# Kernel optimization log

Measured on AMD Instinct MI355X. Metric: run time of the kernel, lower is better.

The kernel has to match this reference:

```python
import jax, jax.numpy as jnp
import numpy as np

N_NODES = 16500   # 100 battles x 165 hexes
N_EDGES = 100000  # per link type
K = 3             # number of link types (HeteroConv branches)
C_IN, C_HID, C_OUT = 170, 256, 256
GEN_EPS = 1e-7    # GENConv eps
BN_EPS = 1e-5     # BatchNorm1d eps


def setup_inputs() -> dict:
    key = jax.random.key(0)
    ki = iter(jax.random.split(key, 32))
    inp = {}
    inp["x"] = jax.random.normal(next(ki), (N_NODES, C_IN), jnp.float32)
    inp["edge_index"] = jax.random.randint(next(ki), (K, 2, N_EDGES), 0, N_NODES, dtype=jnp.int32)
    inp["edge_attr"] = jax.random.normal(next(ki), (K, N_EDGES, 1), jnp.float32)

    def uni(k, fan_in, shape):
        b = float(1.0 / np.sqrt(fan_in))
        return jax.random.uniform(k, shape, jnp.float32, -b, b)

    dims = [(C_IN, C_HID), (C_HID, C_HID), (C_HID, C_OUT)]
    for l, (ci, co) in enumerate(dims):
        inp[f"We{l}"] = uni(next(ki), 1, (K, 1, ci))          # edge encoder Linear(1, ci)
        inp[f"be{l}"] = jnp.zeros((K, ci), jnp.float32)
        inp[f"Wa{l}"] = uni(next(ki), ci, (K, ci, 2 * ci))     # MLP layer 1 (expansion=2)
        inp[f"ba{l}"] = jnp.zeros((K, 2 * ci), jnp.float32)
        inp[f"g{l}"] = jnp.ones((K, 2 * ci), jnp.float32)      # BatchNorm gamma
        inp[f"bt{l}"] = jnp.zeros((K, 2 * ci), jnp.float32)    # BatchNorm beta
        inp[f"Wb{l}"] = uni(next(ki), 2 * ci, (K, 2 * ci, co)) # MLP layer 2
        inp[f"bb{l}"] = jnp.zeros((K, co), jnp.float32)
    return inp


def _genconv(x, src, dst, ea, We, be, Wa, ba, g, bt, Wb, bb):
    """PyG GENConv (aggr='softmax', t=1, eps=1e-7, norm='batch') with self loops."""
    n = x.shape[0]
    loops = jnp.arange(n, dtype=src.dtype)
    src = jnp.concatenate([src, loops])
    dst = jnp.concatenate([dst, loops])
    ea = jnp.concatenate([ea, jnp.ones((n, ea.shape[1]), ea.dtype)], axis=0)
    e = ea @ We + be                           # [E+N, ci] edge encoder
    msg = jax.nn.relu(x[src] + e) + GEN_EPS    # [E+N, ci] message
    # per-destination, per-channel segment softmax aggregation
    mx = jax.ops.segment_max(msg, dst, num_segments=n)
    w = jnp.exp(msg - mx[dst])
    den = jax.ops.segment_sum(w, dst, num_segments=n)
    aggr = jax.ops.segment_sum(msg * w, dst, num_segments=n) / den
    out = aggr + x                             # residual with root node
    # MLP: Linear -> BatchNorm(train stats) -> ReLU -> Linear
    h = out @ Wa + ba
    mu = h.mean(axis=0)
    var = ((h - mu) ** 2).mean(axis=0)
    h = (h - mu) * jax.lax.rsqrt(var + BN_EPS) * g + bt
    h = jax.nn.relu(h)
    return h @ Wb + bb


_conv_k = jax.vmap(_genconv, in_axes=(None, 0, 0, 0, 0, 0, 0, 0, 0, 0, 0, 0))


def _forward(x, edge_index, edge_attr, layers):
    h = x
    for i, p in enumerate(layers):
        # HeteroConv: run GENConv per link type, sum-aggregate over types
        h = _conv_k(h, edge_index[:, 0], edge_index[:, 1], edge_attr, *p).sum(axis=0)
        if i < len(layers) - 1:
            h = jax.nn.leaky_relu(h, 0.01)
    return h


def reference(x, edge_index, edge_attr,
              We0, be0, Wa0, ba0, g0, bt0, Wb0, bb0,
              We1, be1, Wa1, ba1, g1, bt1, Wb1, bb1,
              We2, be2, Wa2, ba2, g2, bt2, Wb2, bb2):
    layers = [(We0, be0, Wa0, ba0, g0, bt0, Wb0, bb0),
              (We1, be1, Wa1, ba1, g1, bt1, Wb1, bb1),
              (We2, be2, Wa2, ba2, g2, bt2, Wb2, bb2)]
    return _forward(x, edge_index, edge_attr, layers)
```

## Files before the change

### kernel.cpp

```cpp
#include <hip/hip_runtime.h>
#include <math.h>

#define NN 16500
#define NP 16512
#define NE 100000
#define KT 3

typedef __attribute__((ext_vector_type(8))) short bf8_t;
typedef __attribute__((ext_vector_type(4))) float f4_t;

__device__ __forceinline__ unsigned short f2bf(float f) {
    unsigned int u = __float_as_uint(f);
    u += 0x7fffu + ((u >> 16) & 1u);
    return (unsigned short)(u >> 16);
}
__device__ __forceinline__ float bf2f(unsigned short h) {
    return __uint_as_float(((unsigned int)h) << 16);
}
__device__ __forceinline__ void gload16(unsigned short* lds, const unsigned short* g) {
    __builtin_amdgcn_global_load_lds(
        (const __attribute__((address_space(1))) void*)g,
        (__attribute__((address_space(3))) void*)lds, 16, 0, 0);
}


__global__ void deg_kernel(const int* __restrict__ ei, int* __restrict__ deg) {
    int t = blockIdx.x * blockDim.x + threadIdx.x;
    if (t >= KT * NE) return;
    int k = t / NE, e = t - k * NE;
    int d = ei[k * 2 * NE + NE + e];
    atomicAdd(&deg[k * NN + d], 1);
}

__global__ void scan_kernel(const int* __restrict__ deg, int* __restrict__ offs,
                            int* __restrict__ cursor) {
    int k = blockIdx.x;
    const int* dg = deg + k * NN;
    int* of = offs + k * (NN + 1);
    int* cu = cursor + k * NN;
    __shared__ int part[256];
    int tid = threadIdx.x;
    const int chunk = (NN + 255) / 256;
    int s0 = tid * chunk, s1 = min(NN, s0 + chunk);
    if (s0 > s1) s0 = s1;
    int sum = 0;
    for (int i = s0; i < s1; ++i) sum += dg[i];
    part[tid] = sum;
    __syncthreads();
    for (int off = 1; off < 256; off <<= 1) {
        int v = part[tid];
        int vp = (tid >= off) ? part[tid - off] : 0;
        __syncthreads();
        part[tid] = v + vp;
        __syncthreads();
    }
    int run = (tid == 0) ? 0 : part[tid - 1];
    for (int i = s0; i < s1; ++i) {
        of[i] = run; cu[i] = run;
        run += dg[i];
    }
    if (tid == 255) of[NN] = run;
}

__global__ void scatter_kernel(const int* __restrict__ ei, int* __restrict__ cursor,
                               int* __restrict__ eids) {
    int t = blockIdx.x * blockDim.x + threadIdx.x;
    if (t >= KT * NE) return;
    int k = t / NE, e = t - k * NE;
    int d = ei[k * 2 * NE + NE + e];
    int pos = atomicAdd(&cursor[k * NN + d], 1);
    eids[k * NE + pos] = e;
}


template<int CI, bool BF16X>
__device__ __forceinline__ void loadrow4(float out[4], const void* xv, int s, int c0) {
    if (BF16X) {
        const unsigned short* xb = (const unsigned short*)xv;
        uint2 u = *(const uint2*)(xb + (size_t)s * CI + c0);
        out[0] = bf2f((unsigned short)(u.x & 0xffffu));
        out[1] = bf2f((unsigned short)(u.x >> 16));
        out[2] = bf2f((unsigned short)(u.y & 0xffffu));
        out[3] = bf2f((unsigned short)(u.y >> 16));
    } else {
        const float* p = (const float*)xv + (size_t)s * CI + c0;
        if (c0 + 4 <= CI) {
            float2 ab = *(const float2*)p;
            float2 cd = *(const float2*)(p + 2);
            out[0] = ab.x; out[1] = ab.y; out[2] = cd.x; out[3] = cd.y;
        } else {
            #pragma unroll
            for (int e = 0; e < 4; ++e) out[e] = (c0 + e < CI) ? p[e] : 0.f;
        }
    }
}

template<int CI, bool BF16X>
__global__ __launch_bounds__(256) void aggr_kernel(
    const void* __restrict__ xv, const int* __restrict__ ei,
    const float* __restrict__ ea_all, const int* __restrict__ offs_all,
    const int* __restrict__ eids_all, const float* __restrict__ We_all,
    const float* __restrict__ be_all,
    unsigned short* __restrict__ out_hi)
{
    constexpr int KP = (CI + 31) / 32 * 32;
    int k = blockIdx.y;
    int wv = threadIdx.x >> 6, lane = threadIdx.x & 63;
    int d = blockIdx.x * 4 + wv;
    int c0 = lane * 4;
    unsigned short* o = out_hi + (size_t)k * NP * KP;
    if (d >= NN) {
        if (c0 < KP) { uint2 z = {0u, 0u}; *(uint2*)(o + (size_t)d * KP + c0) = z; }
        return;
    }
    const int*   src  = ei + (size_t)k * 2 * NE;
    const float* ea   = ea_all + (size_t)k * NE;
    const int*   offs = offs_all + k * (NN + 1);
    const int*   eids = eids_all + (size_t)k * NE;
    const float* We   = We_all + (size_t)k * CI;
    const float* be   = be_all + (size_t)k * CI;

    constexpr bool ACT_ALL = (64 * 4 == KP) && (CI == KP);
    bool act = ACT_ALL || (c0 < CI);
    float w[4], b[4], xd[4] = {0.f, 0.f, 0.f, 0.f};
    #pragma unroll
    for (int e = 0; e < 4; ++e) {
        bool a = (c0 + e) < CI;
        w[e] = a ? We[c0 + e] : 0.f;
        b[e] = a ? be[c0 + e] : 0.f;
    }
    if (act) loadrow4<CI, BF16X>(xd, xv, d, c0);
    #pragma unroll
    for (int e = 0; e < 4; ++e) if ((c0 + e) >= CI) xd[e] = 0.f;

    float m[4], den[4], num[4];
    #pragma unroll
    for (int e = 0; e < 4; ++e) {
        float mg = fmaxf(xd[e] + w[e] + b[e], 0.f);
        m[e] = mg; den[e] = 1.f; num[e] = mg;
    }

    auto step = [&](const float xc[4], float a) {
        #pragma unroll
        for (int e = 0; e < 4; ++e) {
            float t = xc[e] + fmaf(a, w[e], b[e]);
            float mg = fmaxf(t, 0.f);
            float nm = fmaxf(m[e], mg);
            float mn = fminf(m[e], mg);
            float ex = __expf(mn - nm);
            bool keep = m[e] >= mg;
            float e0 = keep ? 1.f : ex;
            float e1 = keep ? ex : 1.f;
            den[e] = fmaf(den[e], e0, e1);
            num[e] = fmaf(num[e], e0, mg * e1);
            m[e] = nm;
        }
    };

    int start = offs[d], end = offs[d + 1];
    for (int base = start; base < end; base += 64) {
        int cnt = min(64, end - base);
        int sv = 0; float av = 0.f;
        if (lane < cnt) {
            int e2 = eids[base + lane];
            sv = src[e2];
            av = ea[e2];
        }
        float x0[4] = {0.f,0.f,0.f,0.f}, x1[4] = {0.f,0.f,0.f,0.f};
        {
            int sA = __shfl(sv, 0);
            if (act) loadrow4<CI, BF16X>(x0, xv, sA, c0);
        }
        if (cnt > 1) {
            int sB = __shfl(sv, 1);
            if (act) loadrow4<CI, BF16X>(x1, xv, sB, c0);
        }
        int j = 0;
        for (; j + 1 < cnt; j += 2) {
            float a0 = __shfl(av, j), a1 = __shfl(av, j + 1);
            float tA[4] = {x0[0], x0[1], x0[2], x0[3]};
            float tB[4] = {x1[0], x1[1], x1[2], x1[3]};
            if (j + 2 < cnt) {
                int sn = __shfl(sv, j + 2);
                if (act) loadrow4<CI, BF16X>(x0, xv, sn, c0);
            }
            if (j + 3 < cnt) {
                int sn = __shfl(sv, j + 3);
                if (act) loadrow4<CI, BF16X>(x1, xv, sn, c0);
            }
            step(tA, a0);
            step(tB, a1);
        }
        if (j < cnt) {
            float a0 = __shfl(av, j);
            step(x0, a0);
        }
    }
    if (c0 < KP) {
        unsigned short r[4];
        #pragma unroll
        for (int e = 0; e < 4; ++e) {
            float v = ((c0 + e) < CI) ? (num[e] / den[e] + xd[e]) : 0.f;
            r[e] = f2bf(v);
        }
        uint2 pk = {(unsigned)r[0] | ((unsigned)r[1] << 16),
                    (unsigned)r[2] | ((unsigned)r[3] << 16)};
        *(uint2*)(o + (size_t)d * KP + c0) = pk;
    }
}


struct SplitJob { const float* W; unsigned short* out; int kdim, ndim, np_, kp; };
struct SplitJobs { SplitJob j[6]; };

__global__ void split_all_kernel(SplitJobs jobs) {
    SplitJob jb = jobs.j[blockIdx.z];
    int idx = blockIdx.x * 256 + threadIdx.x;
    int total = KT * jb.np_ * jb.kp;
    if (idx >= total) return;
    int k = idx / (jb.np_ * jb.kp);
    int rem = idx - k * jb.np_ * jb.kp;
    int n = rem / jb.kp;
    int kk = rem - n * jb.kp;
    float v = (n < jb.ndim && kk < jb.kdim) ? jb.W[((size_t)k * jb.kdim + kk) * jb.ndim + n] : 0.f;
    jb.out[idx] = f2bf(v);
}


__global__ __launch_bounds__(256, 3) void gemm1_mfma(
    const unsigned short* __restrict__ A_hi,
    const unsigned short* __restrict__ B_hi,
    const float* __restrict__ bias_all, unsigned short* __restrict__ C_all,
    float* __restrict__ psum,
    int KP, int ldc, int Mv, int Nv)
{
    __shared__ unsigned short Ah[128 * 32];
    __shared__ unsigned short Bh[128 * 32];

    int z = blockIdx.z;
    int gxT = gridDim.x, gyT = gridDim.y;
    int NHP = gxT * 128;
    const unsigned short* Ahg = A_hi + (size_t)z * NP * KP;
    const unsigned short* Bhg = B_hi + (size_t)z * NHP * KP;
    const float* bias = bias_all + (size_t)z * Nv;
    unsigned short* C = C_all + (size_t)z * NP * ldc;

    int tid = threadIdx.x;
    int w = tid >> 6, l = tid & 63;
    int bm = blockIdx.y * 128, bn = blockIdx.x * 128;
    int lane15 = l & 15, quad = l >> 4;
    int wm = (w >> 1) * 64, wn = (w & 1) * 64;
    int srow = l & 15;
    int scol = (l >> 4) * 8;

    f4_t acc[4][4];
    #pragma unroll
    for (int i = 0; i < 4; ++i)
        #pragma unroll
        for (int j = 0; j < 4; ++j) { f4_t zz = {0.f,0.f,0.f,0.f}; acc[i][j] = zz; }

    size_t aoff0 = (size_t)(bm + 32 * w +  0 + srow) * KP + scol;
    size_t aoff1 = (size_t)(bm + 32 * w + 16 + srow) * KP + scol;
    size_t boff0 = (size_t)(bn + 32 * w +  0 + srow) * KP + scol;
    size_t boff1 = (size_t)(bn + 32 * w + 16 + srow) * KP + scol;
    int rb0 = 32 * w, rb1 = 32 * w + 16;
    int ta = (w >> 1) * 4, tb = (w & 1) * 4;

    for (int k0 = 0; k0 < KP; k0 += 32) {
        gload16(&Ah[rb0 * 32], Ahg + aoff0 + k0);
        gload16(&Ah[rb1 * 32], Ahg + aoff1 + k0);
        gload16(&Bh[rb0 * 32], Bhg + boff0 + k0);
        gload16(&Bh[rb1 * 32], Bhg + boff1 + k0);
        __syncthreads();

        bf8_t fa[4], fb[4];
        #pragma unroll
        for (int i = 0; i < 4; ++i) {
            fa[i] = *(const bf8_t*)&Ah[(ta + i) * 512 + l * 8];
            fb[i] = *(const bf8_t*)&Bh[(tb + i) * 512 + l * 8];
        }
        #pragma unroll
        for (int i = 0; i < 4; ++i)
            #pragma unroll
            for (int j = 0; j < 4; ++j)
                acc[i][j] = __builtin_amdgcn_mfma_f32_16x16x32_bf16(fa[i], fb[j], acc[i][j], 0, 0, 0);
        __syncthreads();
    }

    #pragma unroll
    for (int j = 0; j < 4; ++j) {
        int c = bn + wn + j * 16 + lane15;
        float bc = (c < Nv) ? bias[c] : 0.f;
        float s1 = 0.f, s2 = 0.f;
        #pragma unroll
        for (int i = 0; i < 4; ++i) {
            #pragma unroll
            for (int r5 = 0; r5 < 4; ++r5) {
                int r = bm + wm + i * 16 + quad * 4 + r5;
                float v = acc[i][j][r5] + bc;
                unsigned short q = f2bf(v);
                if (r < Mv && c < Nv) C[(size_t)r * ldc + c] = q;
                bool ok = (r < NN) && (c < Nv);
                float vq = ok ? bf2f(q) : 0.f;
                s1 += vq;
                s2 = fmaf(vq, vq, s2);
            }
        }
        s1 += __shfl_xor(s1, 16); s2 += __shfl_xor(s2, 16);
        s1 += __shfl_xor(s1, 32); s2 += __shfl_xor(s2, 32);
        if (quad == 0) {
            int wrow = w >> 1;
            int col = wn + j * 16 + lane15;
            size_t o = ((((size_t)z * gyT + blockIdx.y) * gxT + blockIdx.x) * 2 + wrow) * 256 + col * 2;
            float2 st = {s1, s2};
            *(float2*)&psum[o] = st;
        }
    }
}


__global__ __launch_bounds__(512) void finalize_kernel(
    const float* __restrict__ psum,
    const float* __restrict__ g_all, const float* __restrict__ bt_all,
    float* __restrict__ scale_all, float* __restrict__ shift_all,
    int hid, int gxT)
{
    int z = blockIdx.x;
    int c = threadIdx.x;
    if (c >= hid) return;
    int gx = c >> 7, col = c & 127;
    double s1 = 0.0, s2 = 0.0;
    for (int gy = 0; gy < NP / 128; ++gy) {
        size_t base = (((size_t)z * (NP / 128) + gy) * gxT + gx) * 2 * 256 + col * 2;
        float2 a  = *(const float2*)&psum[base];
        float2 b2 = *(const float2*)&psum[base + 256];
        s1 += (double)a.x + b2.x;
        s2 += (double)a.y + b2.y;
    }
    double mu = s1 / NN;
    double var = s2 / NN - mu * mu;
    if (var < 0.0) var = 0.0;
    float rs = (float)(1.0 / sqrt(var + 1e-5));
    float sc = rs * g_all[(size_t)z * hid + c];
    scale_all[(size_t)z * 512 + c] = sc;
    shift_all[(size_t)z * 512 + c] = bt_all[(size_t)z * hid + c] - (float)mu * sc;
}


__global__ __launch_bounds__(256, 3) void gemm2_mfma(
    const unsigned short* __restrict__ h_all, const float* __restrict__ scale_all,
    const float* __restrict__ shift_all,
    const unsigned short* __restrict__ B_hi,
    float* __restrict__ P_all, int KP, int hid, int Mv)
{
    __shared__ unsigned short Ah[128 * 32];
    __shared__ unsigned short Bh[128 * 32];

    int z = blockIdx.z;
    const unsigned short* hz = h_all + (size_t)z * NP * KP;
    const float* scl = scale_all + (size_t)z * 512;
    const float* shf = shift_all + (size_t)z * 512;
    const unsigned short* Bhg = B_hi + (size_t)z * 256 * KP;
    float* P = P_all + (size_t)z * NP * 256;

    int tid = threadIdx.x;
    int w = tid >> 6, l = tid & 63;
    int bm = blockIdx.y * 128, bn = blockIdx.x * 128;
    int lane15 = l & 15, quad = l >> 4;
    int wm = (w >> 1) * 64, wn = (w & 1) * 64;
    int srow = l & 15, scol = (l >> 4) * 8;

    f4_t acc[4][4];
    #pragma unroll
    for (int i = 0; i < 4; ++i)
        #pragma unroll
        for (int j = 0; j < 4; ++j) { f4_t zz = {0.f,0.f,0.f,0.f}; acc[i][j] = zz; }

    size_t boff0 = (size_t)(bn + 32 * w +  0 + srow) * KP + scol;
    size_t boff1 = (size_t)(bn + 32 * w + 16 + srow) * KP + scol;
    int rb0 = 32 * w, rb1 = 32 * w + 16;
    int ta = (w >> 1) * 4, tb = (w & 1) * 4;

    for (int k0 = 0; k0 < KP; k0 += 32) {
        gload16(&Bh[rb0 * 32], Bhg + boff0 + k0);
        gload16(&Bh[rb1 * 32], Bhg + boff1 + k0);

        #pragma unroll
        for (int sseg = 0; sseg < 2; ++sseg) {
            int L = sseg * 256 + tid;
            int chunk = (L >> 4) & 3;
            int grow = ((L >> 6) << 4) + (L & 15);
            int c = k0 + chunk * 8;
            uint4 hv = *(const uint4*)(hz + (size_t)(bm + grow) * KP + c);
            float4 s0 = *(const float4*)(scl + c);
            float4 s1 = *(const float4*)(scl + c + 4);
            float4 t0 = *(const float4*)(shf + c);
            float4 t1 = *(const float4*)(shf + c + 4);
            unsigned int uu[4] = {hv.x, hv.y, hv.z, hv.w};
            float ss[8] = {s0.x, s0.y, s0.z, s0.w, s1.x, s1.y, s1.z, s1.w};
            float tt[8] = {t0.x, t0.y, t0.z, t0.w, t1.x, t1.y, t1.z, t1.w};
            bf8_t hi8;
            #pragma unroll
            for (int e = 0; e < 8; ++e) {
                unsigned short hb = (e & 1) ? (unsigned short)(uu[e >> 1] >> 16)
                                            : (unsigned short)(uu[e >> 1] & 0xffffu);
                float x = bf2f(hb);
                float val = (c + e < hid) ? fmaxf(fmaf(x, ss[e], tt[e]), 0.f) : 0.f;
                hi8[e] = (short)f2bf(val);
            }
            *(bf8_t*)&Ah[L * 8] = hi8;
        }
        __syncthreads();

        bf8_t fa[4], fb[4];
        #pragma unroll
        for (int i = 0; i < 4; ++i) {
            fa[i] = *(const bf8_t*)&Ah[(ta + i) * 512 + l * 8];
            fb[i] = *(const bf8_t*)&Bh[(tb + i) * 512 + l * 8];
        }
        #pragma unroll
        for (int i = 0; i < 4; ++i)
            #pragma unroll
            for (int j = 0; j < 4; ++j)
                acc[i][j] = __builtin_amdgcn_mfma_f32_16x16x32_bf16(fa[i], fb[j], acc[i][j], 0, 0, 0);
        __syncthreads();
    }

    #pragma unroll
    for (int i = 0; i < 4; ++i)
        #pragma unroll
        for (int j = 0; j < 4; ++j) {
            int c = bn + wn + j * 16 + lane15;
            #pragma unroll
            for (int r5 = 0; r5 < 4; ++r5) {
                int r = bm + wm + i * 16 + quad * 4 + r5;
                if (r < Mv)
                    P[(size_t)r * 256 + c] = acc[i][j][r5];
            }
        }
}


__global__ __launch_bounds__(256) void reduce_kernel(
    const float* __restrict__ P, const float* __restrict__ bb,
    float* __restrict__ outf, unsigned short* __restrict__ outb,
    int leaky, int as_bf16)
{
    int idx = blockIdx.x * 256 + threadIdx.x;
    if (idx >= NN * 64) return;
    int r = idx >> 6, c = (idx & 63) * 4;
    const float4 p0 = *(const float4*)&P[((size_t)0 * NP + r) * 256 + c];
    const float4 p1 = *(const float4*)&P[((size_t)1 * NP + r) * 256 + c];
    const float4 p2 = *(const float4*)&P[((size_t)2 * NP + r) * 256 + c];
    const float4 b0 = *(const float4*)&bb[c];
    const float4 b1 = *(const float4*)&bb[256 + c];
    const float4 b2 = *(const float4*)&bb[512 + c];
    float v[4] = {p0.x + p1.x + p2.x + b0.x + b1.x + b2.x,
                  p0.y + p1.y + p2.y + b0.y + b1.y + b2.y,
                  p0.z + p1.z + p2.z + b0.z + b1.z + b2.z,
                  p0.w + p1.w + p2.w + b0.w + b1.w + b2.w};
    if (leaky) {
        #pragma unroll
        for (int e = 0; e < 4; ++e) v[e] = (v[e] > 0.f) ? v[e] : 0.01f * v[e];
    }
    if (as_bf16) {
        unsigned int o0 = (unsigned int)f2bf(v[0]) | ((unsigned int)f2bf(v[1]) << 16);
        unsigned int o1 = (unsigned int)f2bf(v[2]) | ((unsigned int)f2bf(v[3]) << 16);
        uint2 o = {o0, o1};
        *(uint2*)&outb[(size_t)r * 256 + c] = o;
    } else {
        float4 o = {v[0], v[1], v[2], v[3]};
        *(float4*)&outf[(size_t)r * 256 + c] = o;
    }
}


extern "C" void kernel_launch(void* const* d_in, const int* in_sizes, int n_in,
                              void* d_out, int out_size, void* d_ws, size_t ws_size,
                              hipStream_t stream)
{
    const float* x  = (const float*)d_in[0];
    const int*   ei = (const int*)d_in[1];
    const float* ea = (const float*)d_in[2];

    char* w = (char*)d_ws;
    auto alloc = [&](size_t bytes) {
        char* p = w;
        w += (bytes + 255) & ~(size_t)255;
        return p;
    };
    int* deg    = (int*)alloc((size_t)KT * NN * 4);
    int* offs   = (int*)alloc((size_t)KT * (NN + 1) * 4);
    int* cursor = (int*)alloc((size_t)KT * NN * 4);
    int* eids   = (int*)alloc((size_t)KT * NE * 4);
    unsigned short* a1_hi = (unsigned short*)alloc((size_t)KT * NP * 256 * 2);
    unsigned short* h3 = (unsigned short*)alloc((size_t)KT * NP * 512 * 2);
    float* partial = (float*)alloc((size_t)KT * NP * 256 * 4);
    unsigned short* bta_l[3];
    unsigned short* btb_l[3];
    for (int l = 0; l < 3; ++l) {
        bta_l[l] = (unsigned short*)alloc((size_t)KT * 512 * 256 * 2);
        btb_l[l] = (unsigned short*)alloc((size_t)KT * 256 * 512 * 2);
    }
    float* psum = (float*)alloc((size_t)KT * (NP / 128) * 4 * 2 * 256 * 4);
    float* scale3 = (float*)alloc((size_t)KT * 512 * 4);
    float* shift3 = (float*)alloc((size_t)KT * 512 * 4);
    unsigned short* bufA = (unsigned short*)alloc((size_t)NN * 256 * 2);
    unsigned short* bufB = (unsigned short*)alloc((size_t)NN * 256 * 2);

    hipMemsetAsync(deg, 0, (size_t)KT * NN * 4, stream);
    int net = KT * NE;
    deg_kernel<<<(net + 255) / 256, 256, 0, stream>>>(ei, deg);
    scan_kernel<<<KT, 256, 0, stream>>>(deg, offs, cursor);
    scatter_kernel<<<(net + 255) / 256, 256, 0, stream>>>(ei, cursor, eids);

    SplitJobs jobs;
    int maxtot = 0;
    for (int l = 0; l < 3; ++l) {
        int ci  = (l == 0) ? 170 : 256;
        int KP1 = (ci + 31) / 32 * 32;
        int hid = 2 * ci;
        int NHP = (hid + 127) / 128 * 128;
        int KP2 = (hid + 31) / 32 * 32;
        jobs.j[2 * l]     = { (const float*)d_in[3 + 8 * l + 2], bta_l[l], ci,  hid, NHP, KP1 };
        jobs.j[2 * l + 1] = { (const float*)d_in[3 + 8 * l + 6], btb_l[l], hid, 256, 256, KP2 };
        maxtot = max(maxtot, KT * NHP * KP1);
        maxtot = max(maxtot, KT * 256 * KP2);
    }
    dim3 gsp((maxtot + 255) / 256, 1, 6);
    split_all_kernel<<<gsp, 256, 0, stream>>>(jobs);

    const void* hin = x;
    for (int l = 0; l < 3; ++l) {
        int ci  = (l == 0) ? 170 : 256;
        int KP1 = (ci + 31) / 32 * 32;
        int hid = 2 * ci;
        int NHP = (hid + 127) / 128 * 128;
        int KP2 = (hid + 31) / 32 * 32;
        const float* We = (const float*)d_in[3 + 8 * l + 0];
        const float* be = (const float*)d_in[3 + 8 * l + 1];
        const float* ba = (const float*)d_in[3 + 8 * l + 3];
        const float* g  = (const float*)d_in[3 + 8 * l + 4];
        const float* bt = (const float*)d_in[3 + 8 * l + 5];
        const float* bb = (const float*)d_in[3 + 8 * l + 7];

        dim3 ga(NP / 4, KT);
        if (l == 0)
            aggr_kernel<170, false><<<ga, 256, 0, stream>>>(hin, ei, ea, offs, eids,
                                                            We, be, a1_hi);
        else
            aggr_kernel<256, true><<<ga, 256, 0, stream>>>(hin, ei, ea, offs, eids,
                                                           We, be, a1_hi);

        dim3 g1(NHP / 128, NP / 128, KT);
        gemm1_mfma<<<g1, 256, 0, stream>>>(a1_hi, bta_l[l], ba, h3, psum, KP1, KP2, NN, hid);

        finalize_kernel<<<KT, 512, 0, stream>>>(psum, g, bt, scale3, shift3, hid, NHP / 128);

        dim3 g2(2, NP / 128, KT);
        gemm2_mfma<<<g2, 256, 0, stream>>>(h3, scale3, shift3, btb_l[l],
                                           partial, KP2, hid, NP);

        unsigned short* outb = (l == 0) ? bufA : bufB;
        reduce_kernel<<<(NN * 64 + 255) / 256, 256, 0, stream>>>(
            partial, bb, (float*)d_out, outb, (l < 2) ? 1 : 0, (l < 2) ? 1 : 0);

        hin = (l < 2) ? (const void*)outb : nullptr;
    }
}
```

Baseline: 697.9 us.

## Fuse GEMM2 with cross-type reduction and pre-gather edge sources/attributes

The second MLP GEMM now loops over all three link types inside one block, with 64x256 tiles. It accumulates the HeteroConv sum in registers and applies bias, leaky ReLU and the bf16 cast in the epilogue. This removes the fp32 partial buffer and the separate reduce kernel. The scatter kernel now writes source ids and edge attributes in CSR order, so the aggregation kernel no longer does an indirect eid lookup. In exchange, the GEMM has fewer blocks (NP/64, about 258) and does a serial K loop three times longer, with a software prefetch of the next A chunk. The epilogue also writes scalar 2-byte stores that are poorly coalesced.

```diff
diff --git a/kernel.cpp b/kernel.cpp
--- a/kernel.cpp
+++ b/kernel.cpp
@@ -62,14 +62,16 @@
     if (tid == 255) of[NN] = run;
 }
 
-__global__ void scatter_kernel(const int* __restrict__ ei, int* __restrict__ cursor,
-                               int* __restrict__ eids) {
+__global__ void scatter_kernel(const int* __restrict__ ei, const float* __restrict__ ea,
+                               int* __restrict__ cursor,
+                               int* __restrict__ srcs, float* __restrict__ eas) {
     int t = blockIdx.x * blockDim.x + threadIdx.x;
     if (t >= KT * NE) return;
     int k = t / NE, e = t - k * NE;
     int d = ei[k * 2 * NE + NE + e];
     int pos = atomicAdd(&cursor[k * NN + d], 1);
-    eids[k * NE + pos] = e;
+    srcs[k * NE + pos] = ei[k * 2 * NE + e];
+    eas[k * NE + pos]  = ea[(size_t)k * NE + e];
 }
 
 
@@ -97,10 +99,10 @@
 
 template<int CI, bool BF16X>
 __global__ __launch_bounds__(256) void aggr_kernel(
-    const void* __restrict__ xv, const int* __restrict__ ei,
-    const float* __restrict__ ea_all, const int* __restrict__ offs_all,
-    const int* __restrict__ eids_all, const float* __restrict__ We_all,
-    const float* __restrict__ be_all,
+    const void* __restrict__ xv,
+    const int* __restrict__ srcs_all, const float* __restrict__ eas_all,
+    const int* __restrict__ offs_all,
+    const float* __restrict__ We_all, const float* __restrict__ be_all,
     unsigned short* __restrict__ out_hi)
 {
     constexpr int KP = (CI + 31) / 32 * 32;
@@ -113,10 +115,9 @@
         if (c0 < KP) { uint2 z = {0u, 0u}; *(uint2*)(o + (size_t)d * KP + c0) = z; }
         return;
     }
-    const int*   src  = ei + (size_t)k * 2 * NE;
-    const float* ea   = ea_all + (size_t)k * NE;
+    const int*   srcs = srcs_all + (size_t)k * NE;
+    const float* eas  = eas_all + (size_t)k * NE;
     const int*   offs = offs_all + k * (NN + 1);
-    const int*   eids = eids_all + (size_t)k * NE;
     const float* We   = We_all + (size_t)k * CI;
     const float* be   = be_all + (size_t)k * CI;
 
@@ -162,9 +163,8 @@
         int cnt = min(64, end - base);
         int sv = 0; float av = 0.f;
         if (lane < cnt) {
-            int e2 = eids[base + lane];
-            sv = src[e2];
-            av = ea[e2];
+            sv = srcs[base + lane];
+            av = eas[base + lane];
         }
         float x0[4] = {0.f,0.f,0.f,0.f}, x1[4] = {0.f,0.f,0.f,0.f};
         {
@@ -347,131 +347,117 @@
 }
 
 
-__global__ __launch_bounds__(256, 3) void gemm2_mfma(
+__global__ __launch_bounds__(256) void gemm2_fused(
     const unsigned short* __restrict__ h_all, const float* __restrict__ scale_all,
-    const float* __restrict__ shift_all,
-    const unsigned short* __restrict__ B_hi,
-    float* __restrict__ P_all, int KP, int hid, int Mv)
+    const float* __restrict__ shift_all, const unsigned short* __restrict__ B_all,
+    const float* __restrict__ bb, float* __restrict__ outf,
+    unsigned short* __restrict__ outb, int KP, int hid, int leaky, int as_bf16)
 {
-    __shared__ unsigned short Ah[128 * 32];
-    __shared__ unsigned short Bh[128 * 32];
-
-    int z = blockIdx.z;
-    const unsigned short* hz = h_all + (size_t)z * NP * KP;
-    const float* scl = scale_all + (size_t)z * 512;
-    const float* shf = shift_all + (size_t)z * 512;
-    const unsigned short* Bhg = B_hi + (size_t)z * 256 * KP;
-    float* P = P_all + (size_t)z * NP * 256;
+    __shared__ unsigned short Ah[64 * 32];
+    __shared__ unsigned short Bh[256 * 32];
 
     int tid = threadIdx.x;
     int w = tid >> 6, l = tid & 63;
-    int bm = blockIdx.y * 128, bn = blockIdx.x * 128;
     int lane15 = l & 15, quad = l >> 4;
-    int wm = (w >> 1) * 64, wn = (w & 1) * 64;
+    int bm = blockIdx.x * 64;
+    int wmt = (w >> 1) * 2;
+    int wnt = (w & 1) * 8;
+
+    int ar16   = (tid & 63) >> 2;
+    int achunk = tid & 3;
+    int atile  = tid >> 6;
+    int arow   = atile * 16 + ar16;
+    int aldst  = atile * 512 + (achunk * 16 + ar16) * 8;
+
     int srow = l & 15, scol = (l >> 4) * 8;
 
-    f4_t acc[4][4];
-    #pragma unroll
-    for (int i = 0; i < 4; ++i)
-        #pragma unroll
-        for (int j = 0; j < 4; ++j) { f4_t zz = {0.f,0.f,0.f,0.f}; acc[i][j] = zz; }
-
-    size_t boff0 = (size_t)(bn + 32 * w +  0 + srow) * KP + scol;
-    size_t boff1 = (size_t)(bn + 32 * w + 16 + srow) * KP + scol;
-    int rb0 = 32 * w, rb1 = 32 * w + 16;
-    int ta = (w >> 1) * 4, tb = (w & 1) * 4;
-
-    for (int k0 = 0; k0 < KP; k0 += 32) {
-        gload16(&Bh[rb0 * 32], Bhg + boff0 + k0);
-        gload16(&Bh[rb1 * 32], Bhg + boff1 + k0);
-
-        #pragma unroll
-        for (int sseg = 0; sseg < 2; ++sseg) {
-            int L = sseg * 256 + tid;
-            int chunk = (L >> 4) & 3;
-            int grow = ((L >> 6) << 4) + (L & 15);
-            int c = k0 + chunk * 8;
-            uint4 hv = *(const uint4*)(hz + (size_t)(bm + grow) * KP + c);
-            float4 s0 = *(const float4*)(scl + c);
-            float4 s1 = *(const float4*)(scl + c + 4);
-            float4 t0 = *(const float4*)(shf + c);
-            float4 t1 = *(const float4*)(shf + c + 4);
-            unsigned int uu[4] = {hv.x, hv.y, hv.z, hv.w};
-            float ss[8] = {s0.x, s0.y, s0.z, s0.w, s1.x, s1.y, s1.z, s1.w};
-            float tt[8] = {t0.x, t0.y, t0.z, t0.w, t1.x, t1.y, t1.z, t1.w};
-            bf8_t hi8;
-            #pragma unroll
-            for (int e = 0; e < 8; ++e) {
-                unsigned short hb = (e & 1) ? (unsigned short)(uu[e >> 1] >> 16)
-                                            : (unsigned short)(uu[e >> 1] & 0xffffu);
-                float x = bf2f(hb);
-                float val = (c + e < hid) ? fmaxf(fmaf(x, ss[e], tt[e]), 0.f) : 0.f;
-                hi8[e] = (short)f2bf(val);
-            }
-            *(bf8_t*)&Ah[L * 8] = hi8;
-        }
-        __syncthreads();
-
-        bf8_t fa[4], fb[4];
-        #pragma unroll
-        for (int i = 0; i < 4; ++i) {
-            fa[i] = *(const bf8_t*)&Ah[(ta + i) * 512 + l * 8];
-            fb[i] = *(const bf8_t*)&Bh[(tb + i) * 512 + l * 8];
-        }
-        #pragma unroll
-        for (int i = 0; i < 4; ++i)
-            #pragma unroll
-            for (int j = 0; j < 4; ++j)
-                acc[i][j] = __builtin_amdgcn_mfma_f32_16x16x32_bf16(fa[i], fb[j], acc[i][j], 0, 0, 0);
-        __syncthreads();
-    }
-
-    #pragma unroll
-    for (int i = 0; i < 4; ++i)
-        #pragma unroll
-        for (int j = 0; j < 4; ++j) {
-            int c = bn + wn + j * 16 + lane15;
+    f4_t acc[2][8];
+    #pragma unroll
+    for (int i = 0; i < 2; ++i)
+        #pragma unroll
+        for (int j = 0; j < 8; ++j) { f4_t zz = {0.f,0.f,0.f,0.f}; acc[i][j] = zz; }
+
+    uint4 hp; float4 sp0, sp1, tp0, tp1;
+    {
+        hp = *(const uint4*)(h_all + (size_t)(bm + arow) * KP + achunk * 8);
+        const float* scl = scale_all;
+        const float* shf = shift_all;
+        int c = achunk * 8;
+        sp0 = *(const float4*)(scl + c); sp1 = *(const float4*)(scl + c + 4);
+        tp0 = *(const float4*)(shf + c); tp1 = *(const float4*)(shf + c + 4);
+    }
+
+    for (int z = 0; z < KT; ++z) {
+        const unsigned short* Bz = B_all + (size_t)z * 256 * KP;
+        for (int k0 = 0; k0 < KP; k0 += 32) {
+            #pragma unroll
+            for (int q = 0; q < 4; ++q) {
+                int n = w * 64 + q * 16 + srow;
+                gload16(&Bh[(w * 4 + q) * 512], Bz + (size_t)n * KP + k0 + scol);
+            }
+            uint4 hv = hp;
+            float4 s0 = sp0, s1 = sp1, t0 = tp0, t1 = tp1;
+            int nk = k0 + 32, nz = z;
+            if (nk >= KP) { nk = 0; nz = z + 1; }
+            if (nz < KT) {
+                const unsigned short* hn = h_all + (size_t)nz * NP * KP;
+                hp = *(const uint4*)(hn + (size_t)(bm + arow) * KP + nk + achunk * 8);
+                const float* scl = scale_all + (size_t)nz * 512;
+                const float* shf = shift_all + (size_t)nz * 512;
+                int c = nk + achunk * 8;
+                sp0 = *(const float4*)(scl + c); sp1 = *(const float4*)(scl + c + 4);
+                tp0 = *(const float4*)(shf + c); tp1 = *(const float4*)(shf + c + 4);
+            }
+            {
+                int c = k0 + achunk * 8;
+                unsigned int uu[4] = {hv.x, hv.y, hv.z, hv.w};
+                float ss[8] = {s0.x, s0.y, s0.z, s0.w, s1.x, s1.y, s1.z, s1.w};
+                float tt[8] = {t0.x, t0.y, t0.z, t0.w, t1.x, t1.y, t1.z, t1.w};
+                bf8_t hi8;
+                #pragma unroll
+                for (int e = 0; e < 8; ++e) {
+                    unsigned short hb = (e & 1) ? (unsigned short)(uu[e >> 1] >> 16)
+                                                : (unsigned short)(uu[e >> 1] & 0xffffu);
+                    float x = bf2f(hb);
+                    float val = (c + e < hid) ? fmaxf(fmaf(x, ss[e], tt[e]), 0.f) : 0.f;
+                    hi8[e] = (short)f2bf(val);
+                }
+                *(bf8_t*)&Ah[aldst] = hi8;
+            }
+            __syncthreads();
+
+            bf8_t fa[2], fb[8];
+            #pragma unroll
+            for (int i = 0; i < 2; ++i)
+                fa[i] = *(const bf8_t*)&Ah[(wmt + i) * 512 + l * 8];
+            #pragma unroll
+            for (int j = 0; j < 8; ++j)
+                fb[j] = *(const bf8_t*)&Bh[(wnt + j) * 512 + l * 8];
+            #pragma unroll
+            for (int i = 0; i < 2; ++i)
+                #pragma unroll
+                for (int j = 0; j < 8; ++j)
+                    acc[i][j] = __builtin_amdgcn_mfma_f32_16x16x32_bf16(fa[i], fb[j], acc[i][j], 0, 0, 0);
+            __syncthreads();
+        }
+    }
+
+    #pragma unroll
+    for (int i = 0; i < 2; ++i)
+        #pragma unroll
+        for (int j = 0; j < 8; ++j) {
+            int c = (w & 1) * 128 + j * 16 + lane15;
+            float bc = bb[c] + bb[256 + c] + bb[512 + c];
             #pragma unroll
             for (int r5 = 0; r5 < 4; ++r5) {
-                int r = bm + wm + i * 16 + quad * 4 + r5;
-                if (r < Mv)
-                    P[(size_t)r * 256 + c] = acc[i][j][r5];
-            }
-        }
-}
-
-
-__global__ __launch_bounds__(256) void reduce_kernel(
-    const float* __restrict__ P, const float* __restrict__ bb,
-    float* __restrict__ outf, unsigned short* __restrict__ outb,
-    int leaky, int as_bf16)
-{
-    int idx = blockIdx.x * 256 + threadIdx.x;
-    if (idx >= NN * 64) return;
-    int r = idx >> 6, c = (idx & 63) * 4;
-    const float4 p0 = *(const float4*)&P[((size_t)0 * NP + r) * 256 + c];
-    const float4 p1 = *(const float4*)&P[((size_t)1 * NP + r) * 256 + c];
-    const float4 p2 = *(const float4*)&P[((size_t)2 * NP + r) * 256 + c];
-    const float4 b0 = *(const float4*)&bb[c];
-    const float4 b1 = *(const float4*)&bb[256 + c];
-    const float4 b2 = *(const float4*)&bb[512 + c];
-    float v[4] = {p0.x + p1.x + p2.x + b0.x + b1.x + b2.x,
-                  p0.y + p1.y + p2.y + b0.y + b1.y + b2.y,
-                  p0.z + p1.z + p2.z + b0.z + b1.z + b2.z,
-                  p0.w + p1.w + p2.w + b0.w + b1.w + b2.w};
-    if (leaky) {
-        #pragma unroll
-        for (int e = 0; e < 4; ++e) v[e] = (v[e] > 0.f) ? v[e] : 0.01f * v[e];
-    }
-    if (as_bf16) {
-        unsigned int o0 = (unsigned int)f2bf(v[0]) | ((unsigned int)f2bf(v[1]) << 16);
-        unsigned int o1 = (unsigned int)f2bf(v[2]) | ((unsigned int)f2bf(v[3]) << 16);
-        uint2 o = {o0, o1};
-        *(uint2*)&outb[(size_t)r * 256 + c] = o;
-    } else {
-        float4 o = {v[0], v[1], v[2], v[3]};
-        *(float4*)&outf[(size_t)r * 256 + c] = o;
-    }
+                int r = bm + (w >> 1) * 32 + i * 16 + quad * 4 + r5;
+                if (r >= NN) continue;
+                float v = acc[i][j][r5] + bc;
+                if (leaky) v = (v > 0.f) ? v : 0.01f * v;
+                if (as_bf16) outb[(size_t)r * 256 + c] = f2bf(v);
+                else         outf[(size_t)r * 256 + c] = v;
+            }
+        }
 }
 
 
@@ -492,10 +478,10 @@
     int* deg    = (int*)alloc((size_t)KT * NN * 4);
     int* offs   = (int*)alloc((size_t)KT * (NN + 1) * 4);
     int* cursor = (int*)alloc((size_t)KT * NN * 4);
-    int* eids   = (int*)alloc((size_t)KT * NE * 4);
+    int* srcs   = (int*)alloc((size_t)KT * NE * 4);
+    float* eas  = (float*)alloc((size_t)KT * NE * 4);
     unsigned short* a1_hi = (unsigned short*)alloc((size_t)KT * NP * 256 * 2);
     unsigned short* h3 = (unsigned short*)alloc((size_t)KT * NP * 512 * 2);
-    float* partial = (float*)alloc((size_t)KT * NP * 256 * 4);
     unsigned short* bta_l[3];
     unsigned short* btb_l[3];
     for (int l = 0; l < 3; ++l) {
@@ -512,7 +498,7 @@
     int net = KT * NE;
     deg_kernel<<<(net + 255) / 256, 256, 0, stream>>>(ei, deg);
     scan_kernel<<<KT, 256, 0, stream>>>(deg, offs, cursor);
-    scatter_kernel<<<(net + 255) / 256, 256, 0, stream>>>(ei, cursor, eids);
+    scatter_kernel<<<(net + 255) / 256, 256, 0, stream>>>(ei, ea, cursor, srcs, eas);
 
     SplitJobs jobs;
     int maxtot = 0;
@@ -546,10 +532,10 @@
 
         dim3 ga(NP / 4, KT);
         if (l == 0)
-            aggr_kernel<170, false><<<ga, 256, 0, stream>>>(hin, ei, ea, offs, eids,
+            aggr_kernel<170, false><<<ga, 256, 0, stream>>>(hin, srcs, eas, offs,
                                                             We, be, a1_hi);
         else
-            aggr_kernel<256, true><<<ga, 256, 0, stream>>>(hin, ei, ea, offs, eids,
+            aggr_kernel<256, true><<<ga, 256, 0, stream>>>(hin, srcs, eas, offs,
                                                            We, be, a1_hi);
 
         dim3 g1(NHP / 128, NP / 128, KT);
@@ -557,13 +543,10 @@
 
         finalize_kernel<<<KT, 512, 0, stream>>>(psum, g, bt, scale3, shift3, hid, NHP / 128);
 
-        dim3 g2(2, NP / 128, KT);
-        gemm2_mfma<<<g2, 256, 0, stream>>>(h3, scale3, shift3, btb_l[l],
-                                           partial, KP2, hid, NP);
-
         unsigned short* outb = (l == 0) ? bufA : bufB;
-        reduce_kernel<<<(NN * 64 + 255) / 256, 256, 0, stream>>>(
-            partial, bb, (float*)d_out, outb, (l < 2) ? 1 : 0, (l < 2) ? 1 : 0);
+        gemm2_fused<<<NP / 64, 256, 0, stream>>>(h3, scale3, shift3, btb_l[l], bb,
+                                                 (float*)d_out, outb, KP2, hid,
+                                                 (l < 2) ? 1 : 0, (l < 2) ? 1 : 0);
 
         hin = (l < 2) ? (const void*)outb : nullptr;
     }
```

Measured after the change: 705.9 us. No clear change (+1.1%).

## Pre-gather edge sources/attrs in CSR, deepen aggr prefetch, store partials in bf16

Applied to the files above, without the earlier changes.

The scatter kernel now writes the source index and edge attribute directly into CSR order, so the aggregation kernel reads them contiguously instead of going through an edge-id indirection. The aggregation loop now keeps four neighbour rows in flight per bank, double-buffered across two banks, instead of two. The gemm2 partial outputs are stored as bf16 rather than fp32, halving the traffic to and from reduce_kernel. The extra prefetch depth raises register pressure, and bf16 partials lose precision before the cross-type sum.

```diff
diff --git a/kernel.cpp b/kernel.cpp
--- a/kernel.cpp
+++ b/kernel.cpp
@@ -62,14 +62,16 @@
     if (tid == 255) of[NN] = run;
 }
 
-__global__ void scatter_kernel(const int* __restrict__ ei, int* __restrict__ cursor,
-                               int* __restrict__ eids) {
+__global__ void scatter_kernel(const int* __restrict__ ei, const float* __restrict__ ea,
+                               int* __restrict__ cursor,
+                               int* __restrict__ srcs, float* __restrict__ eas) {
     int t = blockIdx.x * blockDim.x + threadIdx.x;
     if (t >= KT * NE) return;
     int k = t / NE, e = t - k * NE;
     int d = ei[k * 2 * NE + NE + e];
     int pos = atomicAdd(&cursor[k * NN + d], 1);
-    eids[k * NE + pos] = e;
+    srcs[k * NE + pos] = ei[k * 2 * NE + e];
+    eas[k * NE + pos]  = ea[(size_t)k * NE + e];
 }
 
 
@@ -97,10 +99,10 @@
 
 template<int CI, bool BF16X>
 __global__ __launch_bounds__(256) void aggr_kernel(
-    const void* __restrict__ xv, const int* __restrict__ ei,
-    const float* __restrict__ ea_all, const int* __restrict__ offs_all,
-    const int* __restrict__ eids_all, const float* __restrict__ We_all,
-    const float* __restrict__ be_all,
+    const void* __restrict__ xv,
+    const int* __restrict__ srcs_all, const float* __restrict__ eas_all,
+    const int* __restrict__ offs_all,
+    const float* __restrict__ We_all, const float* __restrict__ be_all,
     unsigned short* __restrict__ out_hi)
 {
     constexpr int KP = (CI + 31) / 32 * 32;
@@ -113,10 +115,9 @@
         if (c0 < KP) { uint2 z = {0u, 0u}; *(uint2*)(o + (size_t)d * KP + c0) = z; }
         return;
     }
-    const int*   src  = ei + (size_t)k * 2 * NE;
-    const float* ea   = ea_all + (size_t)k * NE;
+    const int*   srcs = srcs_all + (size_t)k * NE;
+    const float* eas  = eas_all + (size_t)k * NE;
     const int*   offs = offs_all + k * (NN + 1);
-    const int*   eids = eids_all + (size_t)k * NE;
     const float* We   = We_all + (size_t)k * CI;
     const float* be   = be_all + (size_t)k * CI;
 
@@ -162,38 +163,40 @@
         int cnt = min(64, end - base);
         int sv = 0; float av = 0.f;
         if (lane < cnt) {
-            int e2 = eids[base + lane];
-            sv = src[e2];
-            av = ea[e2];
-        }
-        float x0[4] = {0.f,0.f,0.f,0.f}, x1[4] = {0.f,0.f,0.f,0.f};
-        {
-            int sA = __shfl(sv, 0);
-            if (act) loadrow4<CI, BF16X>(x0, xv, sA, c0);
-        }
-        if (cnt > 1) {
-            int sB = __shfl(sv, 1);
-            if (act) loadrow4<CI, BF16X>(x1, xv, sB, c0);
-        }
+            sv = srcs[base + lane];
+            av = eas[base + lane];
+        }
+        float xq[2][4][4];
+        #pragma unroll
+        for (int t = 0; t < 4; ++t) {
+            #pragma unroll
+            for (int e = 0; e < 4; ++e) xq[0][t][e] = 0.f;
+            if (t < cnt) {
+                int s = __shfl(sv, t);
+                if (act) loadrow4<CI, BF16X>(xq[0][t], xv, s, c0);
+            }
+        }
+        int bank = 0;
         int j = 0;
-        for (; j + 1 < cnt; j += 2) {
-            float a0 = __shfl(av, j), a1 = __shfl(av, j + 1);
-            float tA[4] = {x0[0], x0[1], x0[2], x0[3]};
-            float tB[4] = {x1[0], x1[1], x1[2], x1[3]};
-            if (j + 2 < cnt) {
-                int sn = __shfl(sv, j + 2);
-                if (act) loadrow4<CI, BF16X>(x0, xv, sn, c0);
+        for (; j + 3 < cnt; j += 4) {
+            #pragma unroll
+            for (int t = 0; t < 4; ++t) {
+                if (j + 4 + t < cnt) {
+                    int s = __shfl(sv, j + 4 + t);
+                    if (act) loadrow4<CI, BF16X>(xq[bank ^ 1][t], xv, s, c0);
+                }
             }
-            if (j + 3 < cnt) {
-                int sn = __shfl(sv, j + 3);
-                if (act) loadrow4<CI, BF16X>(x1, xv, sn, c0);
-            }
-            step(tA, a0);
-            step(tB, a1);
-        }
-        if (j < cnt) {
+            float a0 = __shfl(av, j),     a1 = __shfl(av, j + 1);
+            float a2 = __shfl(av, j + 2), a3 = __shfl(av, j + 3);
+            step(xq[bank][0], a0);
+            step(xq[bank][1], a1);
+            step(xq[bank][2], a2);
+            step(xq[bank][3], a3);
+            bank ^= 1;
+        }
+        for (; j < cnt; ++j) {
             float a0 = __shfl(av, j);
-            step(x0, a0);
+            step(xq[bank][j & 3], a0);
         }
     }
     if (c0 < KP) {
@@ -351,7 +354,7 @@
     const unsigned short* __restrict__ h_all, const float* __restrict__ scale_all,
     const float* __restrict__ shift_all,
     const unsigned short* __restrict__ B_hi,
-    float* __restrict__ P_all, int KP, int hid, int Mv)
+    unsigned short* __restrict__ P_all, int KP, int hid, int Mv)
 {
     __shared__ unsigned short Ah[128 * 32];
     __shared__ unsigned short Bh[128 * 32];
@@ -361,7 +364,7 @@
     const float* scl = scale_all + (size_t)z * 512;
     const float* shf = shift_all + (size_t)z * 512;
     const unsigned short* Bhg = B_hi + (size_t)z * 256 * KP;
-    float* P = P_all + (size_t)z * NP * 256;
+    unsigned short* P = P_all + (size_t)z * NP * 256;
 
     int tid = threadIdx.x;
     int w = tid >> 6, l = tid & 63;
@@ -435,33 +438,39 @@
             for (int r5 = 0; r5 < 4; ++r5) {
                 int r = bm + wm + i * 16 + quad * 4 + r5;
                 if (r < Mv)
-                    P[(size_t)r * 256 + c] = acc[i][j][r5];
+                    P[(size_t)r * 256 + c] = f2bf(acc[i][j][r5]);
             }
         }
 }
 
 
 __global__ __launch_bounds__(256) void reduce_kernel(
-    const float* __restrict__ P, const float* __restrict__ bb,
+    const unsigned short* __restrict__ P, const float* __restrict__ bb,
     float* __restrict__ outf, unsigned short* __restrict__ outb,
     int leaky, int as_bf16)
 {
     int idx = blockIdx.x * 256 + threadIdx.x;
     if (idx >= NN * 64) return;
     int r = idx >> 6, c = (idx & 63) * 4;
-    const float4 p0 = *(const float4*)&P[((size_t)0 * NP + r) * 256 + c];
-    const float4 p1 = *(const float4*)&P[((size_t)1 * NP + r) * 256 + c];
-    const float4 p2 = *(const float4*)&P[((size_t)2 * NP + r) * 256 + c];
+    uint2 q0 = *(const uint2*)&P[((size_t)0 * NP + r) * 256 + c];
+    uint2 q1 = *(const uint2*)&P[((size_t)1 * NP + r) * 256 + c];
+    uint2 q2 = *(const uint2*)&P[((size_t)2 * NP + r) * 256 + c];
     const float4 b0 = *(const float4*)&bb[c];
     const float4 b1 = *(const float4*)&bb[256 + c];
     const float4 b2 = *(const float4*)&bb[512 + c];
-    float v[4] = {p0.x + p1.x + p2.x + b0.x + b1.x + b2.x,
-                  p0.y + p1.y + p2.y + b0.y + b1.y + b2.y,
-                  p0.z + p1.z + p2.z + b0.z + b1.z + b2.z,
-                  p0.w + p1.w + p2.w + b0.w + b1.w + b2.w};
-    if (leaky) {
-        #pragma unroll
-        for (int e = 0; e < 4; ++e) v[e] = (v[e] > 0.f) ? v[e] : 0.01f * v[e];
+    float p0[4] = {bf2f((unsigned short)(q0.x & 0xffffu)), bf2f((unsigned short)(q0.x >> 16)),
+                   bf2f((unsigned short)(q0.y & 0xffffu)), bf2f((unsigned short)(q0.y >> 16))};
+    float p1[4] = {bf2f((unsigned short)(q1.x & 0xffffu)), bf2f((unsigned short)(q1.x >> 16)),
+                   bf2f((unsigned short)(q1.y & 0xffffu)), bf2f((unsigned short)(q1.y >> 16))};
+    float p2[4] = {bf2f((unsigned short)(q2.x & 0xffffu)), bf2f((unsigned short)(q2.x >> 16)),
+                   bf2f((unsigned short)(q2.y & 0xffffu)), bf2f((unsigned short)(q2.y >> 16))};
+    float bbs[4] = {b0.x + b1.x + b2.x, b0.y + b1.y + b2.y,
+                    b0.z + b1.z + b2.z, b0.w + b1.w + b2.w};
+    float v[4];
+    #pragma unroll
+    for (int e = 0; e < 4; ++e) {
+        v[e] = p0[e] + p1[e] + p2[e] + bbs[e];
+        if (leaky) v[e] = (v[e] > 0.f) ? v[e] : 0.01f * v[e];
     }
     if (as_bf16) {
         unsigned int o0 = (unsigned int)f2bf(v[0]) | ((unsigned int)f2bf(v[1]) << 16);
@@ -492,10 +501,11 @@
     int* deg    = (int*)alloc((size_t)KT * NN * 4);
     int* offs   = (int*)alloc((size_t)KT * (NN + 1) * 4);
     int* cursor = (int*)alloc((size_t)KT * NN * 4);
-    int* eids   = (int*)alloc((size_t)KT * NE * 4);
+    int* srcs   = (int*)alloc((size_t)KT * NE * 4);
+    float* eas  = (float*)alloc((size_t)KT * NE * 4);
     unsigned short* a1_hi = (unsigned short*)alloc((size_t)KT * NP * 256 * 2);
     unsigned short* h3 = (unsigned short*)alloc((size_t)KT * NP * 512 * 2);
-    float* partial = (float*)alloc((size_t)KT * NP * 256 * 4);
+    unsigned short* partial = (unsigned short*)alloc((size_t)KT * NP * 256 * 2);
     unsigned short* bta_l[3];
     unsigned short* btb_l[3];
     for (int l = 0; l < 3; ++l) {
@@ -512,7 +522,7 @@
     int net = KT * NE;
     deg_kernel<<<(net + 255) / 256, 256, 0, stream>>>(ei, deg);
     scan_kernel<<<KT, 256, 0, stream>>>(deg, offs, cursor);
-    scatter_kernel<<<(net + 255) / 256, 256, 0, stream>>>(ei, cursor, eids);
+    scatter_kernel<<<(net + 255) / 256, 256, 0, stream>>>(ei, ea, cursor, srcs, eas);
 
     SplitJobs jobs;
     int maxtot = 0;
@@ -546,10 +556,10 @@
 
         dim3 ga(NP / 4, KT);
         if (l == 0)
-            aggr_kernel<170, false><<<ga, 256, 0, stream>>>(hin, ei, ea, offs, eids,
+            aggr_kernel<170, false><<<ga, 256, 0, stream>>>(hin, srcs, eas, offs,
                                                             We, be, a1_hi);
         else
-            aggr_kernel<256, true><<<ga, 256, 0, stream>>>(hin, ei, ea, offs, eids,
+            aggr_kernel<256, true><<<ga, 256, 0, stream>>>(hin, srcs, eas, offs,
                                                            We, be, a1_hi);
 
         dim3 g1(NHP / 128, NP / 128, KT);
```

Result: slower. 896.0 us (+28.4%).
